# Kernel tuning notes

Measured on AMD Instinct MI355X. Metric: run time of the kernel, lower is better.

## Reference

```python
import jax, jax.numpy as jnp
import numpy as np

EPS = 1e-6

def setup_inputs() -> dict:
    key = jax.random.key(0)
    k1, k2 = jax.random.split(key)
    S, B, H, F = 2048, 4, 2048, 8192
    x = jax.random.normal(k1, (S, B, H), dtype=jnp.float32)
    scale = jnp.ones((H,), dtype=jnp.float32)
    ln_bias = jnp.zeros((H,), dtype=jnp.float32)
    kernel = jax.random.normal(k2, (H, F), dtype=jnp.float32) * 0.02  # ~variance_scaling fan_in
    return {"x": x, "scale": scale, "ln_bias": ln_bias, "kernel": kernel}

def reference(x, scale, ln_bias, kernel):
    # LayerNorm over last (hidden) axis, stats in fp32
    mu = jnp.mean(x, axis=-1, keepdims=True)
    var = jnp.mean(jnp.square(x - mu), axis=-1, keepdims=True)
    y = (x - mu) * jax.lax.rsqrt(var + EPS) * scale + ln_bias  # [S,B,H]
    # Dense: contract hidden axis against kernel [H,F]
    z = jnp.einsum('sbh,hf->sbf', y, kernel)  # [S,B,F]
    # return_layernorm_output=True -> (dense_out, ln_out)
    return (z, y)
```

## Files before the change

kernel.cpp:

```cpp
#include <hip/hip_runtime.h>
#include <stdint.h>


typedef __attribute__((ext_vector_type(8))) short short8;
typedef __attribute__((ext_vector_type(4))) float floatx4;

__device__ __forceinline__ unsigned short f2bf(float f) {
    unsigned u = __builtin_bit_cast(unsigned, f);
    u += 0x7fffu + ((u >> 16) & 1u);
    return (unsigned short)(u >> 16);
}

__global__ __launch_bounds__(256) void ln_kernel(
    const float* __restrict__ x, const float* __restrict__ scale,
    const float* __restrict__ bias, float* __restrict__ y,
    unsigned short* __restrict__ ybf, int H)
{
    const int row = blockIdx.x;
    const float* xr = x + (size_t)row * H;
    const int tid = threadIdx.x;

    float4 v0 = ((const float4*)xr)[tid];
    float4 v1 = ((const float4*)xr)[tid + 256];

    float s  = v0.x + v0.y + v0.z + v0.w + v1.x + v1.y + v1.z + v1.w;
    float ss = v0.x*v0.x + v0.y*v0.y + v0.z*v0.z + v0.w*v0.w
             + v1.x*v1.x + v1.y*v1.y + v1.z*v1.z + v1.w*v1.w;

    #pragma unroll
    for (int off = 32; off > 0; off >>= 1) {
        s  += __shfl_down(s,  off, 64);
        ss += __shfl_down(ss, off, 64);
    }
    __shared__ float rs[4], rq[4];
    if ((tid & 63) == 0) { rs[tid >> 6] = s; rq[tid >> 6] = ss; }
    __syncthreads();
    float ts = rs[0] + rs[1] + rs[2] + rs[3];
    float tq = rq[0] + rq[1] + rq[2] + rq[3];
    float mean = ts / (float)H;
    float var  = tq / (float)H - mean * mean;
    float rstd = rsqrtf(var + 1e-6f);

    float4 sc0 = ((const float4*)scale)[tid];
    float4 sc1 = ((const float4*)scale)[tid + 256];
    float4 b0  = ((const float4*)bias)[tid];
    float4 b1  = ((const float4*)bias)[tid + 256];

    float4 o0, o1;
    o0.x = (v0.x - mean) * rstd * sc0.x + b0.x;
    o0.y = (v0.y - mean) * rstd * sc0.y + b0.y;
    o0.z = (v0.z - mean) * rstd * sc0.z + b0.z;
    o0.w = (v0.w - mean) * rstd * sc0.w + b0.w;
    o1.x = (v1.x - mean) * rstd * sc1.x + b1.x;
    o1.y = (v1.y - mean) * rstd * sc1.y + b1.y;
    o1.z = (v1.z - mean) * rstd * sc1.z + b1.z;
    o1.w = (v1.w - mean) * rstd * sc1.w + b1.w;

    float* yr = y + (size_t)row * H;
    ((float4*)yr)[tid]       = o0;
    ((float4*)yr)[tid + 256] = o1;

    unsigned short* br = ybf + (size_t)row * H;
    uint2 p0, p1;
    p0.x = (unsigned)f2bf(o0.x) | ((unsigned)f2bf(o0.y) << 16);
    p0.y = (unsigned)f2bf(o0.z) | ((unsigned)f2bf(o0.w) << 16);
    p1.x = (unsigned)f2bf(o1.x) | ((unsigned)f2bf(o1.y) << 16);
    p1.y = (unsigned)f2bf(o1.z) | ((unsigned)f2bf(o1.w) << 16);
    ((uint2*)br)[tid]       = p0;
    ((uint2*)br)[tid + 256] = p1;
}

__global__ __launch_bounds__(256) void transpose_cast_kernel(
    const float* __restrict__ W, unsigned short* __restrict__ Bt,
    int K, int F)
{
    __shared__ float tile[64][65];
    const int kBase = blockIdx.y * 64;
    const int fBase = blockIdx.x * 64;
    const int tid = threadIdx.x;

    #pragma unroll
    for (int p = 0; p < 4; ++p) {
        int kl = (tid >> 4) + p * 16;
        int fl = (tid & 15) * 4;
        float4 v = *(const float4*)&W[(size_t)(kBase + kl) * F + fBase + fl];
        tile[kl][fl]     = v.x;
        tile[kl][fl + 1] = v.y;
        tile[kl][fl + 2] = v.z;
        tile[kl][fl + 3] = v.w;
    }
    __syncthreads();

    #pragma unroll
    for (int p = 0; p < 2; ++p) {
        int fl = (tid >> 3) + p * 32;
        int k8 = (tid & 7) * 8;
        unsigned w[4];
        #pragma unroll
        for (int j = 0; j < 4; ++j) {
            unsigned lo = f2bf(tile[k8 + 2*j][fl]);
            unsigned hi = f2bf(tile[k8 + 2*j + 1][fl]);
            w[j] = lo | (hi << 16);
        }
        uint4 out = make_uint4(w[0], w[1], w[2], w[3]);
        *(uint4*)&Bt[(size_t)(fBase + fl) * K + kBase + k8] = out;
    }
}

#define GBM 256
#define GBN 256
#define GBK 64

__device__ __forceinline__ void stage_half(
    const unsigned short* __restrict__ gA,
    const unsigned short* __restrict__ gB,
    unsigned short* dstA,
    unsigned short* dstB,
    int t, int kh, int K, int tid)
{
    const size_t kb = (size_t)t * GBK + (size_t)kh * 32;
    #pragma unroll
    for (int i = 0; i < 2; ++i) {
        int e  = i * 512 + tid;
        int r  = e >> 2;
        int c2 = (e & 3) ^ ((r >> 2) & 3);
        __builtin_amdgcn_global_load_lds(
            (const __attribute__((address_space(1))) unsigned int*)
                (gA + (size_t)r * K + kb + c2 * 8),
            (__attribute__((address_space(3))) unsigned int*)(dstA + e * 8),
            16, 0, 0);
    }
    #pragma unroll
    for (int i = 0; i < 2; ++i) {
        int e  = i * 512 + tid;
        int r  = e >> 2;
        int c2 = (e & 3) ^ ((r >> 2) & 3);
        __builtin_amdgcn_global_load_lds(
            (const __attribute__((address_space(1))) unsigned int*)
                (gB + (size_t)r * K + kb + c2 * 8),
            (__attribute__((address_space(3))) unsigned int*)(dstB + e * 8),
            16, 0, 0);
    }
}

__device__ __forceinline__ void compute_phase(
    const unsigned short* bufA,
    const unsigned short* bufB,
    floatx4 (&acc)[8][4],
    int waveM, int waveN, int quad, int l16, int sl)
{
    short8 a[8], b[4];
    #pragma unroll
    for (int mi = 0; mi < 8; ++mi) {
        int r = waveM * 128 + mi * 16 + l16;
        a[mi] = *(const short8*)(bufA + ((size_t)r * 4 + sl) * 8);
    }
    #pragma unroll
    for (int ni = 0; ni < 4; ++ni) {
        int r = waveN * 64 + ni * 16 + l16;
        b[ni] = *(const short8*)(bufB + ((size_t)r * 4 + sl) * 8);
    }
    __builtin_amdgcn_s_setprio(1);
    #pragma unroll
    for (int mi = 0; mi < 8; ++mi)
        #pragma unroll
        for (int ni = 0; ni < 4; ++ni)
            acc[mi][ni] = __builtin_amdgcn_mfma_f32_16x16x32_bf16(
                a[mi], b[ni], acc[mi][ni], 0, 0, 0);
    __builtin_amdgcn_s_setprio(0);
}

__global__ __launch_bounds__(512, 2) void gemm_bf16_8w(
    const unsigned short* __restrict__ A,
    const unsigned short* __restrict__ Bt,
    float* __restrict__ C,
    int M, int N, int K)
{
    __shared__ __align__(128) unsigned short lds[2][2][2][8192];

    const int tid   = threadIdx.x;
    const int lane  = tid & 63;
    const int wave  = tid >> 6;
    const int waveM = wave >> 2;
    const int waveN = wave & 3;
    const int quad  = lane >> 4;
    const int l16   = lane & 15;
    const int sl    = quad ^ (l16 >> 2);

    const int nwg = gridDim.x;
    const int cpx = nwg >> 3;
    const int bid = blockIdx.x;
    const int wg  = (bid & 7) * cpx + (bid >> 3);
    const int tilesN = N >> 8;
    const int tm = wg / tilesN;
    const int tn = wg % tilesN;

    const unsigned short* gA = A  + (size_t)tm * GBM * K;
    const unsigned short* gB = Bt + (size_t)tn * GBN * K;

    const int NTt = K >> 6;

    floatx4 acc[8][4] = {};

    stage_half(gA, gB, &lds[0][0][0][0], &lds[0][1][0][0], 0, 0, K, tid);
    stage_half(gA, gB, &lds[0][0][1][0], &lds[0][1][1][0], 0, 1, K, tid);
    stage_half(gA, gB, &lds[1][0][0][0], &lds[1][1][0][0], 1, 0, K, tid);
    asm volatile("s_waitcnt vmcnt(8)" ::: "memory");
    __builtin_amdgcn_s_barrier();

    for (int t = 0; t < NTt; ++t) {
        const int p = t & 1;
        {
            int ts = (t + 1 < NTt) ? (t + 1) : (NTt - 1);
            stage_half(gA, gB, &lds[p ^ 1][0][1][0], &lds[p ^ 1][1][1][0],
                       ts, 1, K, tid);
            compute_phase(&lds[p][0][0][0], &lds[p][1][0][0], acc,
                          waveM, waveN, quad, l16, sl);
            asm volatile("s_waitcnt vmcnt(8)" ::: "memory");
            __builtin_amdgcn_s_barrier();
        }
        {
            int ts = (t + 2 < NTt) ? (t + 2) : (NTt - 1);
            stage_half(gA, gB, &lds[p][0][0][0], &lds[p][1][0][0],
                       ts, 0, K, tid);
            compute_phase(&lds[p][0][1][0], &lds[p][1][1][0], acc,
                          waveM, waveN, quad, l16, sl);
            asm volatile("s_waitcnt vmcnt(8)" ::: "memory");
            __builtin_amdgcn_s_barrier();
        }
    }

    const size_t bm = (size_t)tm * GBM;
    const size_t bn = (size_t)tn * GBN;
    #pragma unroll
    for (int mi = 0; mi < 8; ++mi) {
        #pragma unroll
        for (int ni = 0; ni < 4; ++ni) {
            size_t col = bn + (size_t)waveN * 64 + ni * 16 + l16;
            #pragma unroll
            for (int r = 0; r < 4; ++r) {
                size_t row = bm + (size_t)waveM * 128 + mi * 16 + quad * 4 + r;
                C[row * N + col] = acc[mi][ni][r];
            }
        }
    }
}

extern "C" void kernel_launch(void* const* d_in, const int* in_sizes, int n_in,
                              void* d_out, int out_size, void* d_ws, size_t ws_size,
                              hipStream_t stream) {
    const float* x      = (const float*)d_in[0];
    const float* scale  = (const float*)d_in[1];
    const float* lnbias = (const float*)d_in[2];
    const float* W      = (const float*)d_in[3];

    const int H = in_sizes[1];
    const int M = in_sizes[0] / H;
    const int F = in_sizes[3] / H;

    float* z = (float*)d_out;
    float* y = z + (size_t)M * F;

    unsigned short* Abf = (unsigned short*)d_ws;
    unsigned short* Btb = Abf + (size_t)M * H;

    ln_kernel<<<M, 256, 0, stream>>>(x, scale, lnbias, y, Abf, H);
    transpose_cast_kernel<<<dim3(F / 64, H / 64), 256, 0, stream>>>(W, Btb, H, F);
    gemm_bf16_8w<<<dim3((M / GBM) * (F / GBN)), 512, 0, stream>>>(Abf, Btb, z, M, F, H);
}
```

Measured before the change: 694.0 us.

## Restructure GEMM mainloop into four sub-tile phases with full-tile double buffering

Replaces the half-K staging scheme with full 64-wide K tiles double-buffered in LDS, using a new row layout and an XOR swizzle on 8-element groups. Each K tile is computed in four quadrant phases that reuse loaded A/B fragments across phases and place a barrier around each MFMA cluster, so the waves interleave LDS reads with matrix ops in a ping-pong fashion. The goal is finer-grained overlap of LDS loads, global prefetch and MFMA work, plus fewer LDS reads per K step. The extra barriers per tile add synchronisation overhead, and the new swizzle or buffer indexing may cause bank conflicts or correctness problems.

```diff
diff --git a/kernel.cpp b/kernel.cpp
--- a/kernel.cpp
+++ b/kernel.cpp
@@ -111,63 +111,62 @@
 #define GBN 256
 #define GBK 64
 
-__device__ __forceinline__ void stage_half(
+__device__ __forceinline__ void gload16(const unsigned short* src,
+                                        unsigned short* dst) {
+    __builtin_amdgcn_global_load_lds(
+        (const __attribute__((address_space(1))) unsigned int*)src,
+        (__attribute__((address_space(3))) unsigned int*)dst, 16, 0, 0);
+}
+
+__device__ __forceinline__ void stage_tile(
     const unsigned short* __restrict__ gA,
     const unsigned short* __restrict__ gB,
-    unsigned short* dstA,
-    unsigned short* dstB,
-    int t, int kh, int K, int tid)
-{
-    const size_t kb = (size_t)t * GBK + (size_t)kh * 32;
-    #pragma unroll
-    for (int i = 0; i < 2; ++i) {
-        int e  = i * 512 + tid;
-        int r  = e >> 2;
-        int c2 = (e & 3) ^ ((r >> 2) & 3);
-        __builtin_amdgcn_global_load_lds(
-            (const __attribute__((address_space(1))) unsigned int*)
-                (gA + (size_t)r * K + kb + c2 * 8),
-            (__attribute__((address_space(3))) unsigned int*)(dstA + e * 8),
-            16, 0, 0);
-    }
-    #pragma unroll
-    for (int i = 0; i < 2; ++i) {
-        int e  = i * 512 + tid;
-        int r  = e >> 2;
-        int c2 = (e & 3) ^ ((r >> 2) & 3);
-        __builtin_amdgcn_global_load_lds(
-            (const __attribute__((address_space(1))) unsigned int*)
-                (gB + (size_t)r * K + kb + c2 * 8),
-            (__attribute__((address_space(3))) unsigned int*)(dstB + e * 8),
-            16, 0, 0);
-    }
-}
-
-__device__ __forceinline__ void compute_phase(
-    const unsigned short* bufA,
-    const unsigned short* bufB,
-    floatx4 (&acc)[8][4],
-    int waveM, int waveN, int quad, int l16, int sl)
-{
-    short8 a[8], b[4];
-    #pragma unroll
-    for (int mi = 0; mi < 8; ++mi) {
-        int r = waveM * 128 + mi * 16 + l16;
-        a[mi] = *(const short8*)(bufA + ((size_t)r * 4 + sl) * 8);
-    }
-    #pragma unroll
-    for (int ni = 0; ni < 4; ++ni) {
-        int r = waveN * 64 + ni * 16 + l16;
-        b[ni] = *(const short8*)(bufB + ((size_t)r * 4 + sl) * 8);
-    }
+    unsigned short* dst, int t, int K, int o0, int d0)
+{
+    const int kb = t * GBK;
+    #pragma unroll
+    for (int j = 0; j < 4; ++j)
+        gload16(gA + (size_t)(o0 + j * 64 * K + kb), dst + j * 4096 + d0);
+    #pragma unroll
+    for (int j = 0; j < 4; ++j)
+        gload16(gB + (size_t)(o0 + j * 64 * K + kb), dst + 16384 + j * 4096 + d0);
+}
+
+template<int MH, int NH, bool LA, bool LB>
+__device__ __forceinline__ void quad_phase(
+    const unsigned short* bufA, const unsigned short* bufB,
+    int rowA, int rowB, int s0, int s1,
+    short8 (&a)[4][2], short8 (&b)[2][2], floatx4 (&acc)[8][4])
+{
+    if (LA) {
+        #pragma unroll
+        for (int i = 0; i < 4; ++i) {
+            const unsigned short* rp = bufA + (MH * 64 + i * 16) * 64 + rowA;
+            a[i][0] = *(const short8*)(rp + s0);
+            a[i][1] = *(const short8*)(rp + s1);
+        }
+    }
+    if (LB) {
+        #pragma unroll
+        for (int j = 0; j < 2; ++j) {
+            const unsigned short* rp = bufB + ((NH * 2 + j) * 16) * 64 + rowB;
+            b[j][0] = *(const short8*)(rp + s0);
+            b[j][1] = *(const short8*)(rp + s1);
+        }
+    }
+    __builtin_amdgcn_s_barrier();
     __builtin_amdgcn_s_setprio(1);
     #pragma unroll
-    for (int mi = 0; mi < 8; ++mi)
-        #pragma unroll
-        for (int ni = 0; ni < 4; ++ni)
-            acc[mi][ni] = __builtin_amdgcn_mfma_f32_16x16x32_bf16(
-                a[mi], b[ni], acc[mi][ni], 0, 0, 0);
+    for (int i = 0; i < 4; ++i)
+        #pragma unroll
+        for (int j = 0; j < 2; ++j) {
+            acc[MH*4+i][NH*2+j] = __builtin_amdgcn_mfma_f32_16x16x32_bf16(
+                a[i][0], b[j][0], acc[MH*4+i][NH*2+j], 0, 0, 0);
+            acc[MH*4+i][NH*2+j] = __builtin_amdgcn_mfma_f32_16x16x32_bf16(
+                a[i][1], b[j][1], acc[MH*4+i][NH*2+j], 0, 0, 0);
+        }
     __builtin_amdgcn_s_setprio(0);
+    __builtin_amdgcn_s_barrier();
 }
 
 __global__ __launch_bounds__(512, 2) void gemm_bf16_8w(
@@ -176,7 +175,7 @@
     float* __restrict__ C,
     int M, int N, int K)
 {
-    __shared__ __align__(128) unsigned short lds[2][2][2][8192];
+    __shared__ __align__(128) unsigned short lds[2][32768];
 
     const int tid   = threadIdx.x;
     const int lane  = tid & 63;
@@ -185,7 +184,16 @@
     const int waveN = wave & 3;
     const int quad  = lane >> 4;
     const int l16   = lane & 15;
-    const int sl    = quad ^ (l16 >> 2);
+    const int xs    = l16 & 7;
+    const int s0    = (quad ^ xs) * 8;
+    const int s1    = ((4 | quad) ^ xs) * 8;
+    const int rowA  = l16 * 64;
+    const int rowB  = ((waveN & 1) * 64 + l16) * 64;
+
+    const int r0 = tid >> 3;
+    const int g0 = (tid & 7) ^ (r0 & 7);
+    const int o0 = r0 * K + g0 * 8;
+    const int d0 = tid * 8;
 
     const int nwg = gridDim.x;
     const int cpx = nwg >> 3;
@@ -198,33 +206,37 @@
     const unsigned short* gA = A  + (size_t)tm * GBM * K;
     const unsigned short* gB = Bt + (size_t)tn * GBN * K;
 
-    const int NTt = K >> 6;
+    const int NT = K >> 6;
 
     floatx4 acc[8][4] = {};
-
-    stage_half(gA, gB, &lds[0][0][0][0], &lds[0][1][0][0], 0, 0, K, tid);
-    stage_half(gA, gB, &lds[0][0][1][0], &lds[0][1][1][0], 0, 1, K, tid);
-    stage_half(gA, gB, &lds[1][0][0][0], &lds[1][1][0][0], 1, 0, K, tid);
+    short8 a[4][2], b[2][2];
+
+    unsigned short* bufA0 = &lds[0][0] + waveM * 8192;
+    unsigned short* bufB0 = &lds[0][0] + 16384 + (waveN >> 1) * 8192;
+
+    stage_tile(gA, gB, &lds[0][0], 0, K, o0, d0);
+    stage_tile(gA, gB, &lds[1][0], 1, K, o0, d0);
     asm volatile("s_waitcnt vmcnt(8)" ::: "memory");
     __builtin_amdgcn_s_barrier();
 
-    for (int t = 0; t < NTt; ++t) {
-        const int p = t & 1;
+    for (int t = 0; t < NT; t += 2) {
+        quad_phase<0,0,true ,true >(bufA0, bufB0, rowA, rowB, s0, s1, a, b, acc);
+        quad_phase<0,1,false,true >(bufA0, bufB0, rowA, rowB, s0, s1, a, b, acc);
+        quad_phase<1,1,true ,false>(bufA0, bufB0, rowA, rowB, s0, s1, a, b, acc);
+        quad_phase<1,0,false,true >(bufA0, bufB0, rowA, rowB, s0, s1, a, b, acc);
         {
-            int ts = (t + 1 < NTt) ? (t + 1) : (NTt - 1);
-            stage_half(gA, gB, &lds[p ^ 1][0][1][0], &lds[p ^ 1][1][1][0],
-                       ts, 1, K, tid);
-            compute_phase(&lds[p][0][0][0], &lds[p][1][0][0], acc,
-                          waveM, waveN, quad, l16, sl);
+            int ts = (t + 2 < NT) ? (t + 2) : (NT - 1);
+            stage_tile(gA, gB, &lds[0][0], ts, K, o0, d0);
             asm volatile("s_waitcnt vmcnt(8)" ::: "memory");
             __builtin_amdgcn_s_barrier();
         }
+        quad_phase<0,0,true ,true >(bufA0 + 32768, bufB0 + 32768, rowA, rowB, s0, s1, a, b, acc);
+        quad_phase<0,1,false,true >(bufA0 + 32768, bufB0 + 32768, rowA, rowB, s0, s1, a, b, acc);
+        quad_phase<1,1,true ,false>(bufA0 + 32768, bufB0 + 32768, rowA, rowB, s0, s1, a, b, acc);
+        quad_phase<1,0,false,true >(bufA0 + 32768, bufB0 + 32768, rowA, rowB, s0, s1, a, b, acc);
         {
-            int ts = (t + 2 < NTt) ? (t + 2) : (NTt - 1);
-            stage_half(gA, gB, &lds[p][0][0][0], &lds[p][1][0][0],
-                       ts, 0, K, tid);
-            compute_phase(&lds[p][0][1][0], &lds[p][1][1][0], acc,
-                          waveM, waveN, quad, l16, sl);
+            int ts = (t + 3 < NT) ? (t + 3) : (NT - 1);
+            stage_tile(gA, gB, &lds[1][0], ts, K, o0, d0);
             asm volatile("s_waitcnt vmcnt(8)" ::: "memory");
             __builtin_amdgcn_s_barrier();
         }
```

Result: no change. 705.6 us (+1.7%).
